# Optimization experiments

Hardware: AMD Instinct MI355X
Metric: run time of the kernel (lower is better)

The kernel has to match this reference:

```python
import jax, jax.numpy as jnp
import numpy as np

EMBED = 1024
HIDDEN = 4 * EMBED
NUM_EXPERTS = 8
TOP_K = 2


def setup_inputs() -> dict:
    key = jax.random.key(0)
    k_in, k_w1, k_b1, k_w2, k_b2 = jax.random.split(key, 5)
    s1 = 1.0 / np.sqrt(EMBED)
    s2 = 1.0 / np.sqrt(HIDDEN)
    return {
        "inputs": jax.random.normal(k_in, (8, 4096, EMBED), dtype=jnp.float32),
        "w1": jax.random.uniform(k_w1, (EMBED, HIDDEN), jnp.float32, -s1, s1),
        "b1": jax.random.uniform(k_b1, (HIDDEN,), jnp.float32, -s1, s1),
        "w2": jax.random.uniform(k_w2, (HIDDEN, NUM_EXPERTS), jnp.float32, -s2, s2),
        "b2": jax.random.uniform(k_b2, (NUM_EXPERTS,), jnp.float32, -s2, s2),
    }


def reference(inputs, w1, b1, w2, b2):
    # MLP scorer: [B,S,E] -> [B,S,H] -> [B,S,num_experts]
    h = jax.nn.relu(jnp.einsum("bse,eh->bsh", inputs, w1) + b1)
    score = jnp.einsum("bsh,hn->bsn", h, w2) + b2
    # top-k over expert dim
    _, topk_idx = jax.lax.top_k(score, TOP_K)  # [B,S,K]
    # scatter mask: True at top-k positions
    mask = jax.nn.one_hot(topk_idx, NUM_EXPERTS, dtype=jnp.bool_).any(axis=-2)  # [B,S,N]
    masked = jnp.where(mask, score, -jnp.inf)
    router_output = jax.nn.softmax(masked, axis=-1)
    return router_output, topk_idx
```

## Files before the change

kernel.cpp:

```cpp
#include <hip/hip_runtime.h>

#define T_TOK 32768
#define EDIM  1024
#define HDIM  4096
#define NEXP  8
#define TAU   1.0e-3f
#define MAXR  8192


typedef _Float16 f16x8 __attribute__((ext_vector_type(8)));
typedef _Float16 f16x4 __attribute__((ext_vector_type(4)));
typedef __attribute__((ext_vector_type(4))) float f32x4;
#define MFMA16(a, b, c) __builtin_amdgcn_mfma_f32_16x16x32_f16(a, b, c, 0, 0, 0)

__device__ __forceinline__ void gload16(const void* g, void* l) {
    __builtin_amdgcn_global_load_lds(
        (const __attribute__((address_space(1))) void*)g,
        (__attribute__((address_space(3))) void*)l, 16, 0, 0);
}

__global__ __launch_bounds__(256) void split_x_kernel(
    const float* __restrict__ x, _Float16* __restrict__ hi, int n4)
{
    int i = blockIdx.x * 256 + threadIdx.x;
    int stride = gridDim.x * 256;
    for (; i < n4; i += stride) {
        float4 v = ((const float4*)x)[i];
        f16x4 h;
        h[0] = (_Float16)v.x; h[1] = (_Float16)v.y;
        h[2] = (_Float16)v.z; h[3] = (_Float16)v.w;
        *(f16x4*)&hi[i * 4] = h;
    }
}

__global__ __launch_bounds__(256) void split_w1t_kernel(
    const float* __restrict__ w1, _Float16* __restrict__ thi)
{
    __shared__ float t[64][65];
    const int ht = blockIdx.x;
    const int et = blockIdx.y;
    const int tid = threadIdx.x;
    const int er = tid >> 6, hc = tid & 63;
#pragma unroll
    for (int rr = 0; rr < 16; ++rr) {
        int e = rr * 4 + er;
        t[e][hc] = w1[(size_t)(et * 64 + e) * HDIM + ht * 64 + hc];
    }
    __syncthreads();
    const int hl = tid >> 2, eg = tid & 3;
    size_t base = (size_t)(ht * 64 + hl) * EDIM + et * 64 + eg * 16;
#pragma unroll
    for (int q = 0; q < 4; ++q) {
        f16x4 a;
#pragma unroll
        for (int z = 0; z < 4; ++z) a[z] = (_Float16)t[eg * 16 + q * 4 + z][hl];
        *(f16x4*)&thi[base + q * 4] = a;
    }
}

__global__ __launch_bounds__(256, 3) void mfma_score_kernel(
    const _Float16* __restrict__ xhi, const _Float16* __restrict__ whi,
    const float* __restrict__ b1, const float* __restrict__ w2,
    float* __restrict__ part)
{
    __shared__ __align__(16) _Float16 Ahi[128 * 32];
    __shared__ __align__(16) _Float16 Bhi[128 * 32];

    const int ht = blockIdx.x;
    const int m0 = blockIdx.y * 128;
    const int h0 = ht * 128;
    const int tid = threadIdx.x;
    const int l = tid & 63;
    const int wid = tid >> 6;
    const int wm = wid >> 1, wn = wid & 1;

    const int srow = tid >> 2;
    const int sg = (tid & 3) ^ ((srow >> 1) & 3);
    const size_t xa0 = (size_t)(m0 + srow) * EDIM + sg * 8;
    const size_t xa1 = (size_t)(m0 + 64 + srow) * EDIM + sg * 8;
    const size_t wa0 = (size_t)(h0 + srow) * EDIM + sg * 8;
    const size_t wa1 = (size_t)(h0 + 64 + srow) * EDIM + sg * 8;
    const int ldst = tid * 16;

    const int lrow = l & 15, lslot = l >> 4;
    const int rslot = lslot ^ ((lrow >> 1) & 3);
    const int aoff = (wm * 64 + lrow) * 64 + rslot * 16;
    const int boff = (wn * 64 + lrow) * 64 + rslot * 16;

    f32x4 accA[4][4];
    const f32x4 zz = {0.f, 0.f, 0.f, 0.f};
#pragma unroll
    for (int i = 0; i < 4; ++i)
#pragma unroll
        for (int j = 0; j < 4; ++j) accA[i][j] = zz;

    for (int k0 = 0; k0 < EDIM; k0 += 32) {
        __syncthreads();
        gload16(xhi + xa0 + k0, (char*)Ahi + ldst);
        gload16(xhi + xa1 + k0, (char*)Ahi + 4096 + ldst);
        gload16(whi + wa0 + k0, (char*)Bhi + ldst);
        gload16(whi + wa1 + k0, (char*)Bhi + 4096 + ldst);
        __syncthreads();

        f16x8 ah[4];
#pragma unroll
        for (int mf = 0; mf < 4; ++mf)
            ah[mf] = *(const f16x8*)((const char*)Ahi + aoff + mf * 1024);
#pragma unroll
        for (int nf = 0; nf < 4; ++nf) {
            f16x8 bh = *(const f16x8*)((const char*)Bhi + boff + nf * 1024);
#pragma unroll
            for (int mf = 0; mf < 4; ++mf)
                accA[mf][nf] = MFMA16(ah[mf], bh, accA[mf][nf]);
        }
    }

    float b1r[4], w2r[4][8];
#pragma unroll
    for (int nf = 0; nf < 4; ++nf) {
        int h = h0 + wn * 64 + nf * 16 + lrow;
        b1r[nf] = b1[h];
#pragma unroll
        for (int n = 0; n < 8; ++n) w2r[nf][n] = w2[(size_t)h * NEXP + n];
    }

    const int b0 = l & 1, b1b = (l >> 1) & 1, b2 = (l >> 2) & 1, b3 = (l >> 3) & 1;
    const int regf = (b0 << 1) | b1b;
    const int n0e  = b2 * 4 + b3 * 2;
    float outq[4][2];

#pragma unroll
    for (int q = 0; q < 4; ++q) {
        float v[32];
#pragma unroll
        for (int i = 0; i < 32; ++i) v[i] = 0.f;
#pragma unroll
        for (int reg = 0; reg < 4; ++reg)
#pragma unroll
            for (int nf = 0; nf < 4; ++nf) {
                float hv = fmaxf(accA[q][nf][reg] + b1r[nf], 0.f);
#pragma unroll
                for (int n = 0; n < 8; ++n)
                    v[reg * 8 + n] = fmaf(hv, w2r[nf][n], v[reg * 8 + n]);
            }
        float t1[16];
#pragma unroll
        for (int i = 0; i < 16; ++i) {
            float keep = b0 ? v[i + 16] : v[i];
            float send = b0 ? v[i] : v[i + 16];
            t1[i] = keep + __shfl_xor(send, 1);
        }
        float t2[8];
#pragma unroll
        for (int i = 0; i < 8; ++i) {
            float keep = b1b ? t1[i + 8] : t1[i];
            float send = b1b ? t1[i] : t1[i + 8];
            t2[i] = keep + __shfl_xor(send, 2);
        }
        float t3[4];
#pragma unroll
        for (int i = 0; i < 4; ++i) {
            float keep = b2 ? t2[i + 4] : t2[i];
            float send = b2 ? t2[i] : t2[i + 4];
            t3[i] = keep + __shfl_xor(send, 4);
        }
#pragma unroll
        for (int j = 0; j < 2; ++j) {
            float keep = b3 ? t3[j + 2] : t3[j];
            float send = b3 ? t3[j] : t3[j + 2];
            outq[q][j] = keep + __shfl_xor(send, 8);
        }
    }

    __syncthreads();
    float* red = (float*)Ahi;
    if (wn == 1) {
#pragma unroll
        for (int q = 0; q < 4; ++q) {
            red[(wm * 64 + l) * 8 + q * 2 + 0] = outq[q][0];
            red[(wm * 64 + l) * 8 + q * 2 + 1] = outq[q][1];
        }
    }
    __syncthreads();
    if (wn == 0) {
#pragma unroll
        for (int q = 0; q < 4; ++q) {
            float a = outq[q][0] + red[(wm * 64 + l) * 8 + q * 2 + 0];
            float b = outq[q][1] + red[(wm * 64 + l) * 8 + q * 2 + 1];
            int rl = wm * 64 + q * 16 + lslot * 4 + regf;
            *(float2*)&part[((size_t)ht * T_TOK + m0 + rl) * NEXP + n0e] =
                make_float2(a, b);
        }
    }
}

__global__ void zero_counter_kernel(int* c) {
    if (threadIdx.x == 0 && blockIdx.x == 0) *c = 0;
}

__global__ __launch_bounds__(256) void router_finish_kernel(
    const float* __restrict__ part, const float* __restrict__ b2,
    float* __restrict__ out, int nparts, int* __restrict__ counter,
    int* __restrict__ list)
{
    int t = blockIdx.x * 256 + threadIdx.x;
    if (t >= T_TOK) return;

    float s[NEXP];
#pragma unroll
    for (int n = 0; n < NEXP; ++n) s[n] = 0.f;
    for (int p = 0; p < nparts; ++p) {
        const float* ps = part + (size_t)p * T_TOK * NEXP + (size_t)t * NEXP;
        float4 v0 = *reinterpret_cast<const float4*>(ps);
        float4 v1 = *reinterpret_cast<const float4*>(ps + 4);
        s[0] += v0.x; s[1] += v0.y; s[2] += v0.z; s[3] += v0.w;
        s[4] += v1.x; s[5] += v1.y; s[6] += v1.z; s[7] += v1.w;
    }
#pragma unroll
    for (int n = 0; n < NEXP; ++n) s[n] += b2[n];

    int i1 = 0; float v1 = s[0];
#pragma unroll
    for (int n = 1; n < NEXP; ++n) { if (s[n] > v1) { v1 = s[n]; i1 = n; } }
    int i2 = -1; float v2 = -3.402823466e38f;
#pragma unroll
    for (int n = 0; n < NEXP; ++n) { if (n != i1 && s[n] > v2) { v2 = s[n]; i2 = n; } }
    float v3 = -3.402823466e38f;
#pragma unroll
    for (int n = 0; n < NEXP; ++n) { if (n != i1 && n != i2 && s[n] > v3) v3 = s[n]; }

    if ((v1 - v2) < TAU || (v2 - v3) < TAU) {
        int pos = atomicAdd(counter, 1);
        list[pos] = t;
    }

    float e2 = expf(v2 - v1);
    float denom = 1.f + e2;
    float p1 = 1.f / denom;
    float p2 = e2 / denom;
#pragma unroll
    for (int n = 0; n < NEXP; ++n)
        out[(size_t)t * NEXP + n] = (n == i1) ? p1 : ((n == i2) ? p2 : 0.f);
    out[(size_t)T_TOK * NEXP + (size_t)t * 2 + 0] = (float)i1;
    out[(size_t)T_TOK * NEXP + (size_t)t * 2 + 1] = (float)i2;
}

__global__ __launch_bounds__(256) void gather_x_kernel(
    const float* __restrict__ x, const int* __restrict__ counter,
    const int* __restrict__ list, float* __restrict__ xg)
{
    int cnt = *counter; if (cnt > MAXR) cnt = MAXR;
    for (int g = blockIdx.x; g < cnt; g += gridDim.x) {
        const int t = list[g];
        float4 v = ((const float4*)(x + (size_t)t * EDIM))[threadIdx.x];
        ((float4*)(xg + (size_t)g * EDIM))[threadIdx.x] = v;
    }
}

__global__ __launch_bounds__(256) void refine_gemm_kernel(
    const float* __restrict__ xg, const float* __restrict__ w1,
    const float* __restrict__ b1, const float* __restrict__ w2,
    const int* __restrict__ counter, float* __restrict__ rpart)
{
    int cnt = *counter; if (cnt > MAXR) cnt = MAXR;
    const int m0 = blockIdx.y * 64;
    if (m0 >= cnt) return;
    const int ht = blockIdx.x;
    const int h0 = ht * 128;
    const int tid = threadIdx.x;
    const int tx = tid & 15, ty = tid >> 4;

    __shared__ float xs[16][68];
    __shared__ float wsh[16][128];

    float acc[4][8];
#pragma unroll
    for (int i = 0; i < 4; ++i)
#pragma unroll
        for (int j = 0; j < 8; ++j) acc[i][j] = 0.f;

    const int lk = tid & 15, lt = tid >> 4;
    const int lh = tid & 127, lkg = tid >> 7;

    for (int k0 = 0; k0 < EDIM; k0 += 16) {
        __syncthreads();
#pragma unroll
        for (int r = 0; r < 4; ++r)
            xs[lk][lt + r * 16] = xg[(size_t)(m0 + lt + r * 16) * EDIM + k0 + lk];
#pragma unroll
        for (int r = 0; r < 8; ++r)
            wsh[lkg + r * 2][lh] = w1[(size_t)(k0 + lkg + r * 2) * HDIM + h0 + lh];
        __syncthreads();
#pragma unroll
        for (int k = 0; k < 16; ++k) {
            float a[4], b[8];
#pragma unroll
            for (int i = 0; i < 4; ++i) a[i] = xs[k][ty * 4 + i];
            *reinterpret_cast<float4*>(&b[0]) = *reinterpret_cast<const float4*>(&wsh[k][tx * 8]);
            *reinterpret_cast<float4*>(&b[4]) = *reinterpret_cast<const float4*>(&wsh[k][tx * 8 + 4]);
#pragma unroll
            for (int i = 0; i < 4; ++i)
#pragma unroll
                for (int j = 0; j < 8; ++j)
                    acc[i][j] = fmaf(a[i], b[j], acc[i][j]);
        }
    }

    float sred[4][NEXP];
#pragma unroll
    for (int i = 0; i < 4; ++i) {
        float hv[8];
#pragma unroll
        for (int j = 0; j < 8; ++j)
            hv[j] = fmaxf(acc[i][j] + b1[h0 + tx * 8 + j], 0.f);
#pragma unroll
        for (int n = 0; n < NEXP; ++n) {
            float ssum = 0.f;
#pragma unroll
            for (int j = 0; j < 8; ++j)
                ssum = fmaf(hv[j], w2[(size_t)(h0 + tx * 8 + j) * NEXP + n], ssum);
            sred[i][n] = ssum;
        }
    }
#pragma unroll
    for (int i = 0; i < 4; ++i)
#pragma unroll
        for (int n = 0; n < NEXP; ++n) {
            float v = sred[i][n];
            v += __shfl_xor(v, 1);
            v += __shfl_xor(v, 2);
            v += __shfl_xor(v, 4);
            v += __shfl_xor(v, 8);
            sred[i][n] = v;
        }

    if (tx == 0) {
#pragma unroll
        for (int i = 0; i < 4; ++i) {
            int g = m0 + ty * 4 + i;
            if (g < cnt) {
#pragma unroll
                for (int n = 0; n < NEXP; ++n)
                    rpart[((size_t)g * 32 + ht) * NEXP + n] = sred[i][n];
            }
        }
    }
}

__global__ __launch_bounds__(256) void refine_final_kernel(
    const int* __restrict__ counter, const int* __restrict__ list,
    const float* __restrict__ rpart, const float* __restrict__ b2,
    float* __restrict__ out)
{
    int cnt = *counter; if (cnt > MAXR) cnt = MAXR;
    const int g = blockIdx.x * 256 + threadIdx.x;
    if (g >= cnt) return;
    const int t = list[g];
    float s[NEXP];
#pragma unroll
    for (int n = 0; n < NEXP; ++n) s[n] = b2[n];
    for (int r = 0; r < 32; ++r)
#pragma unroll
        for (int n = 0; n < NEXP; ++n)
            s[n] += rpart[((size_t)g * 32 + r) * NEXP + n];

    int i1 = 0; float v1 = s[0];
#pragma unroll
    for (int n = 1; n < NEXP; ++n) { if (s[n] > v1) { v1 = s[n]; i1 = n; } }
    int i2 = -1; float v2 = -3.402823466e38f;
#pragma unroll
    for (int n = 0; n < NEXP; ++n) { if (n != i1 && s[n] > v2) { v2 = s[n]; i2 = n; } }

    float e2 = expf(v2 - v1);
    float denom = 1.f + e2;
    float p1 = 1.f / denom;
    float p2 = e2 / denom;
#pragma unroll
    for (int n = 0; n < NEXP; ++n)
        out[(size_t)t * NEXP + n] = (n == i1) ? p1 : ((n == i2) ? p2 : 0.f);
    out[(size_t)T_TOK * NEXP + (size_t)t * 2 + 0] = (float)i1;
    out[(size_t)T_TOK * NEXP + (size_t)t * 2 + 1] = (float)i2;
}

#define BM 128
#define BH 128
#define BK 16
#define NHT (HDIM / BH)

__global__ __launch_bounds__(256) void score_gemm_kernel(
    const float* __restrict__ x, const float* __restrict__ w1,
    const float* __restrict__ b1, const float* __restrict__ w2,
    float* __restrict__ dst)
{
    __shared__ float xs[BK][BM + 4];
    __shared__ float wsh[BK][BH];
    __shared__ float w2s[BH * NEXP];
    __shared__ float b1s[BH];

    const int htile = blockIdx.x;
    const int mtile = blockIdx.y;
    const int h0 = htile * BH;
    const int m0 = mtile * BM;
    const int tid = threadIdx.x;
    const int tx = tid & 15;
    const int ty = tid >> 4;

    {
        float4 v = *reinterpret_cast<const float4*>(&w2[(size_t)h0 * NEXP + tid * 4]);
        *reinterpret_cast<float4*>(&w2s[tid * 4]) = v;
        if (tid < BH) b1s[tid] = b1[h0 + tid];
    }

    float acc[8][8];
#pragma unroll
    for (int i = 0; i < 8; ++i)
#pragma unroll
        for (int j = 0; j < 8; ++j) acc[i][j] = 0.f;

    const int e_off = tid & 15;
    const int t_row = tid >> 4;
    const int h_off = tid & 127;
    const int k_off = tid >> 7;

    for (int k0 = 0; k0 < EDIM; k0 += BK) {
        __syncthreads();
#pragma unroll
        for (int r = 0; r < 8; ++r) {
            int tok = t_row + r * 16;
            xs[e_off][tok] = x[(size_t)(m0 + tok) * EDIM + k0 + e_off];
        }
#pragma unroll
        for (int r = 0; r < 8; ++r) {
            int k = k_off + r * 2;
            wsh[k][h_off] = w1[(size_t)(k0 + k) * HDIM + h0 + h_off];
        }
        __syncthreads();
#pragma unroll
        for (int k = 0; k < BK; ++k) {
            float a[8], b[8];
            *reinterpret_cast<float4*>(&a[0]) = *reinterpret_cast<const float4*>(&xs[k][ty * 8]);
            *reinterpret_cast<float4*>(&a[4]) = *reinterpret_cast<const float4*>(&xs[k][ty * 8 + 4]);
            *reinterpret_cast<float4*>(&b[0]) = *reinterpret_cast<const float4*>(&wsh[k][tx * 8]);
            *reinterpret_cast<float4*>(&b[4]) = *reinterpret_cast<const float4*>(&wsh[k][tx * 8 + 4]);
#pragma unroll
            for (int i = 0; i < 8; ++i)
#pragma unroll
                for (int j = 0; j < 8; ++j)
                    acc[i][j] = fmaf(a[i], b[j], acc[i][j]);
        }
    }

    float sred[8][NEXP];
#pragma unroll
    for (int i = 0; i < 8; ++i) {
        float hv[8];
#pragma unroll
        for (int j = 0; j < 8; ++j)
            hv[j] = fmaxf(acc[i][j] + b1s[tx * 8 + j], 0.f);
#pragma unroll
        for (int n = 0; n < NEXP; ++n) {
            float ssum = 0.f;
#pragma unroll
            for (int j = 0; j < 8; ++j)
                ssum = fmaf(hv[j], w2s[(tx * 8 + j) * NEXP + n], ssum);
            sred[i][n] = ssum;
        }
    }
#pragma unroll
    for (int i = 0; i < 8; ++i)
#pragma unroll
        for (int n = 0; n < NEXP; ++n) {
            float v = sred[i][n];
            v += __shfl_xor(v, 1);
            v += __shfl_xor(v, 2);
            v += __shfl_xor(v, 4);
            v += __shfl_xor(v, 8);
            sred[i][n] = v;
        }

    if (tx == 0) {
        float* slice = dst + (size_t)htile * T_TOK * NEXP;
#pragma unroll
        for (int i = 0; i < 8; ++i)
#pragma unroll
            for (int n = 0; n < NEXP; ++n)
                slice[(size_t)(m0 + ty * 8 + i) * NEXP + n] = sred[i][n];
    }
}

__global__ __launch_bounds__(256) void finish_simple_kernel(
    const float* __restrict__ part, const float* __restrict__ b2,
    float* __restrict__ out, int nparts)
{
    int t = blockIdx.x * 256 + threadIdx.x;
    if (t >= T_TOK) return;
    float s[NEXP];
#pragma unroll
    for (int n = 0; n < NEXP; ++n) s[n] = 0.f;
    for (int p = 0; p < nparts; ++p) {
        const float* ps = part + (size_t)p * T_TOK * NEXP + (size_t)t * NEXP;
        float4 v0 = *reinterpret_cast<const float4*>(ps);
        float4 v1 = *reinterpret_cast<const float4*>(ps + 4);
        s[0] += v0.x; s[1] += v0.y; s[2] += v0.z; s[3] += v0.w;
        s[4] += v1.x; s[5] += v1.y; s[6] += v1.z; s[7] += v1.w;
    }
#pragma unroll
    for (int n = 0; n < NEXP; ++n) s[n] += b2[n];
    int i1 = 0; float v1 = s[0];
#pragma unroll
    for (int n = 1; n < NEXP; ++n) { if (s[n] > v1) { v1 = s[n]; i1 = n; } }
    int i2 = -1; float v2 = -3.402823466e38f;
#pragma unroll
    for (int n = 0; n < NEXP; ++n) { if (n != i1 && s[n] > v2) { v2 = s[n]; i2 = n; } }
    float e2 = expf(v2 - v1);
    float denom = 1.f + e2;
    float p1 = 1.f / denom;
    float p2 = e2 / denom;
#pragma unroll
    for (int n = 0; n < NEXP; ++n)
        out[(size_t)t * NEXP + n] = (n == i1) ? p1 : ((n == i2) ? p2 : 0.f);
    out[(size_t)T_TOK * NEXP + (size_t)t * 2 + 0] = (float)i1;
    out[(size_t)T_TOK * NEXP + (size_t)t * 2 + 1] = (float)i2;
}

extern "C" void kernel_launch(void* const* d_in, const int* in_sizes, int n_in,
                              void* d_out, int out_size, void* d_ws, size_t ws_size,
                              hipStream_t stream)
{
    const float* x  = (const float*)d_in[0];
    const float* w1 = (const float*)d_in[1];
    const float* b1 = (const float*)d_in[2];
    const float* w2 = (const float*)d_in[3];
    const float* b2 = (const float*)d_in[4];
    float* out = (float*)d_out;

    char* ws = (char*)d_ws;
    _Float16* xhi = (_Float16*)ws;
    _Float16* whi = (_Float16*)(ws + 67108864);
    float* part   = (float*)(ws + 75497472);
    int* counter  = (int*)(ws + 109051904);
    int* list     = (int*)(ws + 109052928);
    float* xg     = (float*)(ws + 109184000);
    float* rpart  = (float*)(ws + 142738432);
    const size_t NEED = 151127040;

    if (ws_size >= NEED) {
        split_x_kernel<<<2048, 256, 0, stream>>>(x, xhi, (T_TOK * EDIM) / 4);
        dim3 tg(64, 16);
        split_w1t_kernel<<<tg, 256, 0, stream>>>(w1, whi);
        dim3 gg(32, 256);
        mfma_score_kernel<<<gg, 256, 0, stream>>>(xhi, whi, b1, w2, part);
        zero_counter_kernel<<<1, 64, 0, stream>>>(counter);
        router_finish_kernel<<<T_TOK / 256, 256, 0, stream>>>(part, b2, out, 32,
                                                              counter, list);
        gather_x_kernel<<<256, 256, 0, stream>>>(x, counter, list, xg);
        dim3 rg(32, MAXR / 64);
        refine_gemm_kernel<<<rg, 256, 0, stream>>>(xg, w1, b1, w2, counter, rpart);
        refine_final_kernel<<<MAXR / 256, 256, 0, stream>>>(counter, list, rpart,
                                                            b2, out);
    } else {
        float* p1 = (float*)d_ws;
        dim3 grid(NHT, T_TOK / BM);
        score_gemm_kernel<<<grid, 256, 0, stream>>>(x, w1, b1, w2, p1);
        finish_simple_kernel<<<T_TOK / 256, 256, 0, stream>>>(p1, b2, out, NHT);
    }
}
```

Before: 671.9 us.

## Triple-buffer LDS loads in score GEMM and remap blocks for XCD locality

```diff
diff --git a/kernel.cpp b/kernel.cpp
--- a/kernel.cpp
+++ b/kernel.cpp
@@ -63,11 +63,14 @@
     const float* __restrict__ b1, const float* __restrict__ w2,
     float* __restrict__ part)
 {
-    __shared__ __align__(16) _Float16 Ahi[128 * 32];
-    __shared__ __align__(16) _Float16 Bhi[128 * 32];
-
-    const int ht = blockIdx.x;
-    const int m0 = blockIdx.y * 128;
+    __shared__ __align__(16) _Float16 A3[3 * 4096];
+    __shared__ __align__(16) _Float16 B3[3 * 4096];
+
+    const int bid = blockIdx.x;
+    const int lg  = (bid & 7) * 1024 + (bid >> 3);
+    const int ht  = (lg >> 10) * 4 + (lg & 3);
+    const int mt  = (lg & 1023) >> 2;
+    const int m0 = mt * 128;
     const int h0 = ht * 128;
     const int tid = threadIdx.x;
     const int l = tid & 63;
@@ -94,26 +97,52 @@
 #pragma unroll
         for (int j = 0; j < 4; ++j) accA[i][j] = zz;
 
-    for (int k0 = 0; k0 < EDIM; k0 += 32) {
-        __syncthreads();
-        gload16(xhi + xa0 + k0, (char*)Ahi + ldst);
-        gload16(xhi + xa1 + k0, (char*)Ahi + 4096 + ldst);
-        gload16(whi + wa0 + k0, (char*)Bhi + ldst);
-        gload16(whi + wa1 + k0, (char*)Bhi + 4096 + ldst);
-        __syncthreads();
-
+    auto stage = [&](int s, int bb) {
+        const int k0 = s * 32;
+        gload16(xhi + xa0 + k0, (char*)A3 + bb * 8192 + ldst);
+        gload16(xhi + xa1 + k0, (char*)A3 + bb * 8192 + 4096 + ldst);
+        gload16(whi + wa0 + k0, (char*)B3 + bb * 8192 + ldst);
+        gload16(whi + wa1 + k0, (char*)B3 + bb * 8192 + 4096 + ldst);
+    };
+    auto compute = [&](int bb) {
+        const char* Ab = (const char*)A3 + bb * 8192;
+        const char* Bb = (const char*)B3 + bb * 8192;
         f16x8 ah[4];
 #pragma unroll
         for (int mf = 0; mf < 4; ++mf)
-            ah[mf] = *(const f16x8*)((const char*)Ahi + aoff + mf * 1024);
+            ah[mf] = *(const f16x8*)(Ab + aoff + mf * 1024);
+        __builtin_amdgcn_s_setprio(1);
 #pragma unroll
         for (int nf = 0; nf < 4; ++nf) {
-            f16x8 bh = *(const f16x8*)((const char*)Bhi + boff + nf * 1024);
+            f16x8 bh = *(const f16x8*)(Bb + boff + nf * 1024);
 #pragma unroll
             for (int mf = 0; mf < 4; ++mf)
                 accA[mf][nf] = MFMA16(ah[mf], bh, accA[mf][nf]);
         }
-    }
+        __builtin_amdgcn_s_setprio(0);
+    };
+
+#define WAITV4 do { asm volatile("s_waitcnt vmcnt(4)" ::: "memory"); \
+                    __builtin_amdgcn_sched_barrier(0); } while (0)
+#define WAITV0 do { asm volatile("s_waitcnt vmcnt(0)" ::: "memory"); \
+                    __builtin_amdgcn_sched_barrier(0); } while (0)
+#define BARR   do { __builtin_amdgcn_s_barrier(); \
+                    __builtin_amdgcn_sched_barrier(0); } while (0)
+
+    stage(0, 0);
+    stage(1, 1);
+
+    for (int t = 0; t < 30; t += 3) {
+        WAITV4; BARR; stage(t + 2, (t + 2) % 3); compute(0);
+        WAITV4; BARR; stage(t + 3, (t + 3) % 3); compute(1);
+        WAITV4; BARR; stage(t + 4, (t + 4) % 3); compute(2);
+    }
+    WAITV4; BARR; compute(0);
+    WAITV0; BARR; compute(1);
+
+#undef WAITV4
+#undef WAITV0
+#undef BARR
 
     float b1r[4], w2r[4][8];
 #pragma unroll
@@ -173,7 +202,7 @@
     }
 
     __syncthreads();
-    float* red = (float*)Ahi;
+    float* red = (float*)A3;
     if (wn == 1) {
 #pragma unroll
         for (int q = 0; q < 4; ++q) {
@@ -548,8 +577,7 @@
         split_x_kernel<<<2048, 256, 0, stream>>>(x, xhi, (T_TOK * EDIM) / 4);
         dim3 tg(64, 16);
         split_w1t_kernel<<<tg, 256, 0, stream>>>(w1, whi);
-        dim3 gg(32, 256);
-        mfma_score_kernel<<<gg, 256, 0, stream>>>(xhi, whi, b1, w2, part);
+        mfma_score_kernel<<<8192, 256, 0, stream>>>(xhi, whi, b1, w2, part);
         zero_counter_kernel<<<1, 64, 0, stream>>>(counter);
         router_finish_kernel<<<T_TOK / 256, 256, 0, stream>>>(part, b2, out, 32,
                                                               counter, list);
```

After: 609.2 us. -9.3%, faster.
